# Kernel optimization log

Hardware: AMD Instinct MI355X
Metric: run time of the kernel (lower is better)

Reference implementation:

```python
import jax, jax.numpy as jnp
import numpy as np
import math

D_MODEL = 1024
N_HEADS = 16
D_HEAD = D_MODEL // N_HEADS
B, T = 2, 2048


def setup_inputs() -> dict:
    key = jax.random.key(0)
    ks = jax.random.split(key, 5)
    x = jax.random.normal(ks[0], (B, T, D_MODEL), dtype=jnp.float32)
    W_qkv = jax.random.normal(ks[1], (D_MODEL, 3 * D_MODEL), dtype=jnp.float32) * 0.02
    b_qkv = jnp.zeros((3 * D_MODEL,), dtype=jnp.float32)
    W_g = jax.random.normal(ks[2], (N_HEADS, D_HEAD, D_HEAD), dtype=jnp.float32) * 0.02
    W_out = jax.random.normal(ks[3], (D_MODEL, D_MODEL), dtype=jnp.float32) * 0.02
    b_out = jnp.zeros((D_MODEL,), dtype=jnp.float32)
    return {"x": x, "W_qkv": W_qkv, "b_qkv": b_qkv, "W_g": W_g, "W_out": W_out, "b_out": b_out}


def reference(x, W_qkv, b_qkv, W_g, W_out, b_out):
    b, t, d = x.shape
    h, dh = N_HEADS, D_HEAD
    qkv = x @ W_qkv + b_qkv                         # (B,T,3D)
    q, k, v = jnp.split(qkv, 3, axis=-1)
    # (B,T,D) -> (B,H,T,dh)
    q = q.reshape(b, t, h, dh).transpose(0, 2, 1, 3)
    k = k.reshape(b, t, h, dh).transpose(0, 2, 1, 3)
    v = v.reshape(b, t, h, dh).transpose(0, 2, 1, 3)
    scale = 1.0 / math.sqrt(dh)
    scores = jnp.einsum('bhtd,bhsd->bhts', q, k) * scale   # (B,H,T,T)
    causal = jnp.tril(jnp.ones((t, t), dtype=bool))
    scores = jnp.where(causal, scores, jnp.float32(-jnp.inf))
    attn = jax.nn.softmax(scores, axis=-1)
    # query-conditioned bilinear value gate (applied at each position)
    g = jax.nn.sigmoid(jnp.einsum('bhtd,hde->bhte', q, W_g))  # (B,H,T,dh)
    v = g * v
    out = jnp.einsum('bhts,bhsd->bhtd', attn, v)             # (B,H,T,dh)
    out = out.transpose(0, 2, 1, 3).reshape(b, t, d)
    return out @ W_out + b_out
```

## Files before the change

### kernel.cpp

```cpp
#include <hip/hip_runtime.h>
#include <hip/hip_bf16.h>

typedef unsigned short ushortT;
typedef __bf16 bf16x8 __attribute__((ext_vector_type(8)));
typedef __bf16 bf16x4 __attribute__((ext_vector_type(4)));
typedef float f32x4 __attribute__((ext_vector_type(4)));

#define T_SEQ 2048
#define DH 64
#define NH 16
#define DM 1024
#define TD 3072
#define BATCH 2
#define LOG2E 1.44269504f

#define BARRIER()   asm volatile("s_barrier" ::: "memory")
#define VMCNT(n)    asm volatile("s_waitcnt vmcnt(" #n ")" ::: "memory")

__device__ inline ushortT f2bf(float f){
    union { float f; unsigned int u; } a; a.f = f;
    unsigned int r = a.u + 0x7fffu + ((a.u >> 16) & 1u);
    return (ushortT)(r >> 16);
}
__device__ inline float bf2f(ushortT u){
    union { float f; unsigned int u; } a; a.u = ((unsigned int)u) << 16;
    return a.f;
}

__device__ inline void gload_lds16(const void* g, void* l){
    __builtin_amdgcn_global_load_lds((const __attribute__((address_space(1))) void*)g,
                                     (__attribute__((address_space(3))) void*)l, 16, 0, 0);
}

__global__ __launch_bounds__(256) void cast_bf16_kernel(const float* __restrict__ in,
                                                        ushortT* __restrict__ out, int n){
    int i = (blockIdx.x * 256 + threadIdx.x) * 4;
    if (i < n){
        float4 v = *(const float4*)&in[i];
        out[i+0] = f2bf(v.x); out[i+1] = f2bf(v.y);
        out[i+2] = f2bf(v.z); out[i+3] = f2bf(v.w);
    }
}

__global__ __launch_bounds__(256) void transcast_kernel(const float* __restrict__ in,
                                                        ushortT* __restrict__ out, int K, int N){
    __shared__ float tile[64][65];
    int n0 = blockIdx.x * 64, k0 = blockIdx.y * 64;
    int tid = threadIdx.x;
    int c  = tid & 63;
    int r4 = tid >> 6;
#pragma unroll
    for (int i = 0; i < 16; i++){
        int k = r4 + i * 4;
        tile[k][c] = in[(size_t)(k0 + k) * N + n0 + c];
    }
    __syncthreads();
#pragma unroll
    for (int i = 0; i < 16; i++){
        int n = r4 + i * 4;
        out[(size_t)(n0 + n) * K + k0 + c] = f2bf(tile[c][n]);
    }
}

__global__ __launch_bounds__(256) void wg_transcast_kernel(const float* __restrict__ in,
                                                           ushortT* __restrict__ out){
    __shared__ float tile[64][65];
    int h = blockIdx.x;
    int tid = threadIdx.x;
    int c = tid & 63, r4 = tid >> 6;
#pragma unroll
    for (int i = 0; i < 16; i++){
        int d = r4 + i*4;
        tile[d][c] = in[h*4096 + d*64 + c];
    }
    __syncthreads();
#pragma unroll
    for (int i = 0; i < 16; i++){
        int e = r4 + i*4;
        out[h*4096 + e*64 + c] = f2bf(tile[c][e]);
    }
}

__device__ inline void store_out(ushortT* C, size_t i, float v){ C[i] = f2bf(v); }
__device__ inline void store_out(float*   C, size_t i, float v){ C[i] = v; }

template <typename OUT>
__global__ __launch_bounds__(256) void gemm_bf16_kernel(const ushortT* __restrict__ A,
                                                        const ushortT* __restrict__ BT,
                                                        const float* __restrict__ bias,
                                                        OUT* __restrict__ C,
                                                        int M, int N, int K){
    __shared__ __align__(16) ushortT As[2][128*32];
    __shared__ __align__(16) ushortT Bs[2][128*32];
    int tid = threadIdx.x;
    int m0 = blockIdx.x * 128;
    int n0 = blockIdx.y * 128;
    int wid = tid >> 6, lane = tid & 63;
    int l15 = lane & 15, g = lane >> 4;
    int wr = wid >> 1, wc = wid & 1;

    f32x4 acc[4][4];
#pragma unroll
    for (int i = 0; i < 4; i++)
#pragma unroll
        for (int j = 0; j < 4; j++) acc[i][j] = (f32x4){0.f,0.f,0.f,0.f};

    int srow = wid * 32 + (lane >> 2);
    int sch  = lane & 3;

#define GSTAGE(buf, k0)                                                                  \
    {                                                                                    \
        _Pragma("unroll")                                                                \
        for (int i_ = 0; i_ < 2; i_++){                                                  \
            int row_ = srow + i_ * 16;                                                   \
            const ushortT* asrc_ = A  + (size_t)(m0 + row_) * K + (k0) + sch * 8;        \
            const ushortT* bsrc_ = BT + (size_t)(n0 + row_) * K + (k0) + sch * 8;        \
            gload_lds16(asrc_, (char*)As[buf] + (wid*2 + i_) * 1024);                    \
            gload_lds16(bsrc_, (char*)Bs[buf] + (wid*2 + i_) * 1024);                    \
        }                                                                                \
    }

    GSTAGE(0, 0);

    int nk = K >> 5;
    for (int kt = 0; kt < nk; kt++){
        int buf = kt & 1;
        BARRIER();
        if (kt + 1 < nk){
            GSTAGE(buf ^ 1, (kt + 1) * 32);
            VMCNT(4);
        } else {
            VMCNT(0);
        }
        BARRIER();

        bf16x8 af[4], bfr[4];
#pragma unroll
        for (int mi = 0; mi < 4; mi++){
            int r = wr*64 + mi*16 + l15;
            af[mi]  = *(const bf16x8*)(As[buf] + r*32 + g*8);
        }
#pragma unroll
        for (int ni = 0; ni < 4; ni++){
            int r = wc*64 + ni*16 + l15;
            bfr[ni] = *(const bf16x8*)(Bs[buf] + r*32 + g*8);
        }
#pragma unroll
        for (int mi = 0; mi < 4; mi++)
#pragma unroll
            for (int ni = 0; ni < 4; ni++)
                acc[mi][ni] = __builtin_amdgcn_mfma_f32_16x16x32_bf16(af[mi], bfr[ni], acc[mi][ni], 0, 0, 0);
    }
#undef GSTAGE

#pragma unroll
    for (int mi = 0; mi < 4; mi++){
#pragma unroll
        for (int jj = 0; jj < 4; jj++){
            int mm = m0 + wr*64 + mi*16 + 4*g + jj;
#pragma unroll
            for (int ni = 0; ni < 4; ni++){
                int nn = n0 + wc*64 + ni*16 + l15;
                float v = acc[mi][ni][jj] + bias[nn];
                store_out(C, (size_t)mm * N + nn, v);
            }
        }
    }
}

__global__ __launch_bounds__(256) void gate_kernel(const ushortT* __restrict__ qkv,
                                                   const ushortT* __restrict__ WgT,
                                                   ushortT* __restrict__ vgT){
    __shared__ __align__(16) ushortT VT[64][72];
    int tblk = blockIdx.x, bh = blockIdx.y;
    int b = bh >> 4, h = bh & 15;
    int tid = threadIdx.x, wid = tid >> 6, lane = tid & 63;
    int l15 = lane & 15, g = lane >> 4;
    int t0 = tblk * 64;
    int tl = wid*16 + l15;

    const ushortT* qrow = qkv + ((size_t)b*T_SEQ + t0 + tl)*TD + h*DH;
    bf16x8 qf0 = *(const bf16x8*)(qrow + 8*g);
    bf16x8 qf1 = *(const bf16x8*)(qrow + 32 + 8*g);

    const ushortT* wbase = WgT + h*4096;
    const ushortT* vrow = qkv + ((size_t)b*T_SEQ + t0 + tl)*TD + 2*DM + h*DH;

#pragma unroll
    for (int ns = 0; ns < 4; ns++){
        int e = ns*16 + l15;
        bf16x8 wf0 = *(const bf16x8*)(wbase + e*64 + 8*g);
        bf16x8 wf1 = *(const bf16x8*)(wbase + e*64 + 32 + 8*g);
        f32x4 z = (f32x4){0.f,0.f,0.f,0.f};
        z = __builtin_amdgcn_mfma_f32_16x16x32_bf16(wf0, qf0, z, 0, 0, 0);
        z = __builtin_amdgcn_mfma_f32_16x16x32_bf16(wf1, qf1, z, 0, 0, 0);
        union { ushortT u[4]; uint2 v; } v4;
        v4.v = *(const uint2*)(vrow + ns*16 + 4*g);
#pragma unroll
        for (int jj = 0; jj < 4; jj++){
            float ex = __builtin_amdgcn_exp2f(-z[jj] * LOG2E);
            float gv = __builtin_amdgcn_rcpf(1.f + ex);
            VT[ns*16 + 4*g + jj][tl] = f2bf(gv * bf2f(v4.u[jj]));
        }
    }
    __syncthreads();
    for (int i = tid; i < 64*8; i += 256){
        int e = i >> 3, c8 = (i & 7) * 8;
        *(uint4*)&vgT[((size_t)bh * DH + e) * T_SEQ + t0 + c8] = *(const uint4*)&VT[e][c8];
    }
}

struct QS {
    bf16x8 qf0, qf1;
    float m_, lsum;
    f32x4 acc[4];
};

__device__ __forceinline__ void softmax_state(f32x4* s, QS& S, bool diag,
                                              int wid, int l15, int g,
                                              bf16x8& pa0, bf16x8& pa1){
    float tmax = -INFINITY;
    if (diag){
        int qrel = wid*16 + l15;
#pragma unroll
        for (int ns = 0; ns < 4; ns++){
            int kbase = ((ns & 2) << 4) + 8*g + ((ns & 1) << 2);
#pragma unroll
            for (int jj = 0; jj < 4; jj++){
                if (kbase + jj > qrel) s[ns][jj] = -INFINITY;
                tmax = fmaxf(tmax, s[ns][jj]);
            }
        }
    } else {
#pragma unroll
        for (int ns = 0; ns < 4; ns++){
            float a = fmaxf(s[ns][0], s[ns][1]);
            float c = fmaxf(s[ns][2], s[ns][3]);
            tmax = fmaxf(tmax, fmaxf(a, c));
        }
    }
    tmax = fmaxf(tmax, __shfl_xor(tmax, 16, 64));
    tmax = fmaxf(tmax, __shfl_xor(tmax, 32, 64));

    float mnew = fmaxf(S.m_, tmax);
    float mc = mnew * LOG2E;
    float rs = 0.f;
#pragma unroll
    for (int jj = 0; jj < 4; jj++){
        float p0 = __builtin_amdgcn_exp2f(fmaf(s[0][jj], LOG2E, -mc));
        float p1 = __builtin_amdgcn_exp2f(fmaf(s[1][jj], LOG2E, -mc));
        float p2 = __builtin_amdgcn_exp2f(fmaf(s[2][jj], LOG2E, -mc));
        float p3 = __builtin_amdgcn_exp2f(fmaf(s[3][jj], LOG2E, -mc));
        rs += (p0 + p1) + (p2 + p3);
        pa0[jj]   = (__bf16)p0;
        pa0[4+jj] = (__bf16)p1;
        pa1[jj]   = (__bf16)p2;
        pa1[4+jj] = (__bf16)p3;
    }
    rs += __shfl_xor(rs, 16, 64);
    rs += __shfl_xor(rs, 32, 64);

    if (!__all(mnew == S.m_)){
        float alpha = __builtin_amdgcn_exp2f(fmaf(S.m_, LOG2E, -mc));
#pragma unroll
        for (int nt = 0; nt < 4; nt++)
#pragma unroll
            for (int jj = 0; jj < 4; jj++) S.acc[nt][jj] *= alpha;
        S.lsum *= alpha;
        S.m_ = mnew;
    }
    S.lsum += rs;
}

__device__ __forceinline__ void proc_tile1(const ushortT* __restrict__ Kb,
                                           const ushortT* __restrict__ Vb,
                                           QS& S, bool diag,
                                           int wid, int l15, int g){
    int l7 = l15 & 7;
    f32x4 s[4];
    __builtin_amdgcn_s_setprio(1);
#pragma unroll
    for (int ns = 0; ns < 4; ns++){
        int kr = ns*16 + l15;
        bf16x8 kf0 = *(const bf16x8*)(Kb + kr*64 + ((g    ) ^ l7)*8);
        bf16x8 kf1 = *(const bf16x8*)(Kb + kr*64 + ((4 + g) ^ l7)*8);
        f32x4 z = (f32x4){0.f,0.f,0.f,0.f};
        z = __builtin_amdgcn_mfma_f32_16x16x32_bf16(kf0, S.qf0, z, 0, 0, 0);
        z = __builtin_amdgcn_mfma_f32_16x16x32_bf16(kf1, S.qf1, z, 0, 0, 0);
        s[ns] = z;
    }
    __builtin_amdgcn_s_setprio(0);

    bf16x8 pa0, pa1;
    softmax_state(s, S, diag, wid, l15, g, pa0, pa1);

    __builtin_amdgcn_s_setprio(1);
#pragma unroll
    for (int ks = 0; ks < 2; ks++){
        bf16x8 pa = ks ? pa1 : pa0;
#pragma unroll
        for (int nt = 0; nt < 4; nt++){
            bf16x8 vf = *(const bf16x8*)(Vb + (nt*16 + l15)*64 + ((ks*4 + g) ^ l7)*8);
            S.acc[nt] = __builtin_amdgcn_mfma_f32_16x16x32_bf16(vf, pa, S.acc[nt], 0, 0, 0);
        }
    }
    __builtin_amdgcn_s_setprio(0);
}

__global__ __launch_bounds__(256, 4) void attn_kernel(const ushortT* __restrict__ qkv,
                                                      const ushortT* __restrict__ vgT,
                                                      ushortT* __restrict__ obf){
    __shared__ __align__(16) ushortT Ks[2][64*64];
    __shared__ __align__(16) ushortT Vs[2][64*64];
    int id = blockIdx.x;
    int bh = id & 31;
    int y  = id >> 5;
    int ya = y & 7, yb = y >> 3;
    int qblk = yb*8 + ((yb & 1) ? 7 - ya : ya);
    int b = bh >> 4, h = bh & 15;
    int tid = threadIdx.x, wid = tid >> 6, lane = tid & 63;
    int l15 = lane & 15, g = lane >> 4;

    const ushortT* Kg = qkv + (size_t)b * T_SEQ * TD + DM + h * DH;
    const ushortT* Vg = vgT + (size_t)bh * DH * T_SEQ;

    int st_row0 = wid*8 + (lane >> 3);
    int st_c    = (lane & 7) ^ ((lane >> 3) & 7);

#define STAGE_TILE(bufidx, kv0)                                                          \
    {                                                                                    \
        _Pragma("unroll")                                                                \
        for (int i_ = 0; i_ < 2; i_++){                                                  \
            int row_  = st_row0 + i_*32;                                                 \
            int prow_ = (row_ & 0x20) | ((row_ & 0x0C) << 1) |                           \
                        ((row_ & 0x10) >> 2) | (row_ & 3);                               \
            const ushortT* ksrc_ = Kg + (size_t)((kv0) + prow_) * TD + st_c*8;           \
            const ushortT* vsrc_ = Vg + (size_t)row_ * T_SEQ + (kv0) + st_c*8;           \
            gload_lds16(ksrc_, (char*)Ks[bufidx] + wid*1024 + i_*4096);                  \
            gload_lds16(vsrc_, (char*)Vs[bufidx] + wid*1024 + i_*4096);                  \
        }                                                                                \
    }

    QS S;
    {
        int qrow = qblk*64 + wid*16 + l15;
        const ushortT* qb = qkv + ((size_t)b * T_SEQ + qrow) * TD + h * DH;
        S.qf0 = *(const bf16x8*)(qb + 8*g);
        S.qf1 = *(const bf16x8*)(qb + 32 + 8*g);
#pragma unroll
        for (int j = 0; j < 8; j++){
            S.qf0[j] = (__bf16)((float)S.qf0[j] * 0.125f);
            S.qf1[j] = (__bf16)((float)S.qf1[j] * 0.125f);
        }
        S.m_ = -INFINITY; S.lsum = 0.f;
#pragma unroll
        for (int nt = 0; nt < 4; nt++) S.acc[nt] = (f32x4){0.f,0.f,0.f,0.f};
    }

    STAGE_TILE(0, 0);

    for (int t = 0; t <= qblk; t++){
        int buf = t & 1;
        BARRIER();
        if (t < qblk){
            STAGE_TILE(buf ^ 1, (t+1)*64);
            VMCNT(4);
        } else {
            VMCNT(0);
        }
        BARRIER();
        proc_tile1(Ks[buf], Vs[buf], S, t == qblk, wid, l15, g);
    }
#undef STAGE_TILE

    float inv = 1.f / S.lsum;
    size_t orow = ((size_t)b * T_SEQ + qblk*64 + wid*16 + l15) * DM + h*DH;
#pragma unroll
    for (int nt = 0; nt < 4; nt++){
        union { ushortT u[4]; uint2 v; } pk;
#pragma unroll
        for (int jj = 0; jj < 4; jj++) pk.u[jj] = f2bf(S.acc[nt][jj] * inv);
        *(uint2*)&obf[orow + nt*16 + 4*g] = pk.v;
    }
}

extern "C" void kernel_launch(void* const* d_in, const int* in_sizes, int n_in,
                              void* d_out, int out_size, void* d_ws, size_t ws_size,
                              hipStream_t stream){
    const float* x    = (const float*)d_in[0];
    const float* Wqkv = (const float*)d_in[1];
    const float* bqkv = (const float*)d_in[2];
    const float* Wg   = (const float*)d_in[3];
    const float* Wout = (const float*)d_in[4];
    const float* bout = (const float*)d_in[5];

    char* ws = (char*)d_ws;
    ushortT* xbf   = (ushortT*)(ws);
    ushortT* wqkvT = (ushortT*)(ws + 8388608);
    ushortT* woutT = (ushortT*)(ws + 14680064);
    ushortT* qkvb  = (ushortT*)(ws + 16777216);
    ushortT* vgT   = (ushortT*)(ws + 41943040);
    ushortT* obf   = (ushortT*)(ws + 50331648);
    ushortT* wgT   = (ushortT*)(ws + 58720256);

    cast_bf16_kernel<<<4096, 256, 0, stream>>>(x, xbf, 4194304);
    transcast_kernel<<<dim3(48,16), 256, 0, stream>>>(Wqkv, wqkvT, 1024, 3072);
    transcast_kernel<<<dim3(16,16), 256, 0, stream>>>(Wout, woutT, 1024, 1024);
    wg_transcast_kernel<<<16, 256, 0, stream>>>(Wg, wgT);
    gemm_bf16_kernel<ushortT><<<dim3(32,24), 256, 0, stream>>>(xbf, wqkvT, bqkv, qkvb, 4096, 3072, 1024);
    gate_kernel<<<dim3(32,32), 256, 0, stream>>>(qkvb, wgT, vgT);
    attn_kernel<<<1024, 256, 0, stream>>>(qkvb, vgT, obf);
    gemm_bf16_kernel<float><<<dim3(32,8), 256, 0, stream>>>(obf, woutT, bout, (float*)d_out, 4096, 1024, 1024);
}
```

Baseline: 125.5 us.

## Split KV tiles across two wave groups per block and merge softmax states

The attention kernel now launches 512 threads per block, with two groups of four waves. Each group processes alternating 64-key tiles for the same query block, and the two partial flash-attention states are merged through LDS at the end. This halves the serial KV loop length per block to cut latency on long causal rows. The cost is doubled LDS, an extra merge and barrier, and wasted loads when the tile count is odd, since the last tile is clamped and loaded twice.

```diff
diff --git a/kernel.cpp b/kernel.cpp
--- a/kernel.cpp
+++ b/kernel.cpp
@@ -217,11 +217,11 @@
 };
 
 __device__ __forceinline__ void softmax_state(f32x4* s, QS& S, bool diag,
-                                              int wid, int l15, int g,
+                                              int wq, int l15, int g,
                                               bf16x8& pa0, bf16x8& pa1){
     float tmax = -INFINITY;
     if (diag){
-        int qrel = wid*16 + l15;
+        int qrel = wq*16 + l15;
 #pragma unroll
         for (int ns = 0; ns < 4; ns++){
             int kbase = ((ns & 2) << 4) + 8*g + ((ns & 1) << 2);
@@ -275,7 +275,7 @@
 __device__ __forceinline__ void proc_tile1(const ushortT* __restrict__ Kb,
                                            const ushortT* __restrict__ Vb,
                                            QS& S, bool diag,
-                                           int wid, int l15, int g){
+                                           int wq, int l15, int g){
     int l7 = l15 & 7;
     f32x4 s[4];
     __builtin_amdgcn_s_setprio(1);
@@ -292,7 +292,7 @@
     __builtin_amdgcn_s_setprio(0);
 
     bf16x8 pa0, pa1;
-    softmax_state(s, S, diag, wid, l15, g, pa0, pa1);
+    softmax_state(s, S, diag, wq, l15, g, pa0, pa1);
 
     __builtin_amdgcn_s_setprio(1);
 #pragma unroll
@@ -307,11 +307,11 @@
     __builtin_amdgcn_s_setprio(0);
 }
 
-__global__ __launch_bounds__(256, 4) void attn_kernel(const ushortT* __restrict__ qkv,
+__global__ __launch_bounds__(512, 4) void attn_kernel(const ushortT* __restrict__ qkv,
                                                       const ushortT* __restrict__ vgT,
                                                       ushortT* __restrict__ obf){
-    __shared__ __align__(16) ushortT Ks[2][64*64];
-    __shared__ __align__(16) ushortT Vs[2][64*64];
+    __shared__ __align__(16) ushortT Ks[2][2][64*64];
+    __shared__ __align__(16) ushortT Vs[2][2][64*64];
     int id = blockIdx.x;
     int bh = id & 31;
     int y  = id >> 5;
@@ -320,30 +320,35 @@
     int b = bh >> 4, h = bh & 15;
     int tid = threadIdx.x, wid = tid >> 6, lane = tid & 63;
     int l15 = lane & 15, g = lane >> 4;
+    int grp = wid >> 2;
+    int wq  = wid & 3;
 
     const ushortT* Kg = qkv + (size_t)b * T_SEQ * TD + DM + h * DH;
     const ushortT* Vg = vgT + (size_t)bh * DH * T_SEQ;
 
-    int st_row0 = wid*8 + (lane >> 3);
-    int st_c    = (lane & 7) ^ ((lane >> 3) & 7);
-
-#define STAGE_TILE(bufidx, kv0)                                                          \
+    int st_row  = tid >> 3;
+    int st_c    = (tid & 7) ^ (st_row & 7);
+    int st_prow = (st_row & 0x20) | ((st_row & 0x0C) << 1) |
+                  ((st_row & 0x10) >> 2) | (st_row & 3);
+
+#define STAGE_PAIR(buf, rr)                                                              \
     {                                                                                    \
-        _Pragma("unroll")                                                                \
-        for (int i_ = 0; i_ < 2; i_++){                                                  \
-            int row_  = st_row0 + i_*32;                                                 \
-            int prow_ = (row_ & 0x20) | ((row_ & 0x0C) << 1) |                           \
-                        ((row_ & 0x10) >> 2) | (row_ & 3);                               \
-            const ushortT* ksrc_ = Kg + (size_t)((kv0) + prow_) * TD + st_c*8;           \
-            const ushortT* vsrc_ = Vg + (size_t)row_ * T_SEQ + (kv0) + st_c*8;           \
-            gload_lds16(ksrc_, (char*)Ks[bufidx] + wid*1024 + i_*4096);                  \
-            gload_lds16(vsrc_, (char*)Vs[bufidx] + wid*1024 + i_*4096);                  \
-        }                                                                                \
+        int keT_ = 2*(rr);     if (keT_ > qblk) keT_ = qblk;                             \
+        int koT_ = 2*(rr) + 1; if (koT_ > qblk) koT_ = qblk;                             \
+        int kvE_ = keT_ * 64, kvO_ = koT_ * 64;                                          \
+        gload_lds16(Kg + (size_t)(kvE_ + st_prow) * TD + st_c*8,                         \
+                    (char*)Ks[buf][0] + wid*1024);                                       \
+        gload_lds16(Kg + (size_t)(kvO_ + st_prow) * TD + st_c*8,                         \
+                    (char*)Ks[buf][1] + wid*1024);                                       \
+        gload_lds16(Vg + (size_t)st_row * T_SEQ + kvE_ + st_c*8,                         \
+                    (char*)Vs[buf][0] + wid*1024);                                       \
+        gload_lds16(Vg + (size_t)st_row * T_SEQ + kvO_ + st_c*8,                         \
+                    (char*)Vs[buf][1] + wid*1024);                                       \
     }
 
     QS S;
     {
-        int qrow = qblk*64 + wid*16 + l15;
+        int qrow = qblk*64 + wq*16 + l15;
         const ushortT* qb = qkv + ((size_t)b * T_SEQ + qrow) * TD + h * DH;
         S.qf0 = *(const bf16x8*)(qb + 8*g);
         S.qf1 = *(const bf16x8*)(qb + 32 + 8*g);
@@ -357,30 +362,57 @@
         for (int nt = 0; nt < 4; nt++) S.acc[nt] = (f32x4){0.f,0.f,0.f,0.f};
     }
 
-    STAGE_TILE(0, 0);
-
-    for (int t = 0; t <= qblk; t++){
-        int buf = t & 1;
+    int nr = (qblk >> 1) + 1;
+    STAGE_PAIR(0, 0);
+
+    for (int r = 0; r < nr; r++){
+        int buf = r & 1;
         BARRIER();
-        if (t < qblk){
-            STAGE_TILE(buf ^ 1, (t+1)*64);
+        if (r + 1 < nr){
+            STAGE_PAIR(buf ^ 1, r + 1);
             VMCNT(4);
         } else {
             VMCNT(0);
         }
         BARRIER();
-        proc_tile1(Ks[buf], Vs[buf], S, t == qblk, wid, l15, g);
-    }
-#undef STAGE_TILE
-
-    float inv = 1.f / S.lsum;
-    size_t orow = ((size_t)b * T_SEQ + qblk*64 + wid*16 + l15) * DM + h*DH;
-#pragma unroll
-    for (int nt = 0; nt < 4; nt++){
-        union { ushortT u[4]; uint2 v; } pk;
-#pragma unroll
-        for (int jj = 0; jj < 4; jj++) pk.u[jj] = f2bf(S.acc[nt][jj] * inv);
-        *(uint2*)&obf[orow + nt*16 + 4*g] = pk.v;
+        int t = 2*r + grp;
+        if (t <= qblk)
+            proc_tile1(Ks[buf][grp], Vs[buf][grp], S, t == qblk, wq, l15, g);
+    }
+#undef STAGE_PAIR
+
+    BARRIER();
+    float* accL = (float*)&Ks[0][0][0];
+    float* mlL  = (float*)&Vs[0][0][0];
+    if (grp == 1){
+        mlL[(wq*2 + 0)*16 + l15] = S.m_;
+        mlL[(wq*2 + 1)*16 + l15] = S.lsum;
+#pragma unroll
+        for (int nt = 0; nt < 4; nt++)
+#pragma unroll
+            for (int jj = 0; jj < 4; jj++)
+                accL[wq*1024 + (nt*16 + 4*g + jj)*16 + l15] = S.acc[nt][jj];
+    }
+    BARRIER();
+    if (grp == 0){
+        float m2 = mlL[(wq*2 + 0)*16 + l15];
+        float l2 = mlL[(wq*2 + 1)*16 + l15];
+        float mm = fmaxf(S.m_, m2);
+        float a1 = __builtin_amdgcn_exp2f((S.m_ - mm) * LOG2E);
+        float a2 = __builtin_amdgcn_exp2f((m2  - mm) * LOG2E);
+        float inv = 1.f / (S.lsum * a1 + l2 * a2);
+        float ia1 = a1 * inv, ia2 = a2 * inv;
+        size_t orow = ((size_t)b * T_SEQ + qblk*64 + wq*16 + l15) * DM + h*DH;
+#pragma unroll
+        for (int nt = 0; nt < 4; nt++){
+            union { ushortT u[4]; uint2 v; } pk;
+#pragma unroll
+            for (int jj = 0; jj < 4; jj++){
+                float o2 = accL[wq*1024 + (nt*16 + 4*g + jj)*16 + l15];
+                pk.u[jj] = f2bf(S.acc[nt][jj] * ia1 + o2 * ia2);
+            }
+            *(uint2*)&obf[orow + nt*16 + 4*g] = pk.v;
+        }
     }
 }
 
@@ -409,6 +441,6 @@
     wg_transcast_kernel<<<16, 256, 0, stream>>>(Wg, wgT);
     gemm_bf16_kernel<ushortT><<<dim3(32,24), 256, 0, stream>>>(xbf, wqkvT, bqkv, qkvb, 4096, 3072, 1024);
     gate_kernel<<<dim3(32,32), 256, 0, stream>>>(qkvb, wgT, vgT);
-    attn_kernel<<<1024, 256, 0, stream>>>(qkvb, vgT, obf);
+    attn_kernel<<<1024, 512, 0, stream>>>(qkvb, vgT, obf);
     gemm_bf16_kernel<float><<<dim3(32,8), 256, 0, stream>>>(obf, woutT, bout, (float*)d_out, 4096, 1024, 1024);
 }
```

New measurement: 124.7 us. About the same (-0.6%).
